# Kernel optimization log

Measured on AMD Instinct MI355X. Metric: run time of the kernel, lower is better.

Reference implementation:

```python
import jax, jax.numpy as jnp
import numpy as np

B, T, I, H, O = 64, 512, 512, 1024, 128
EPS = 1e-5

def _uniform(key, shape, bound):
    return jax.random.uniform(key, shape, jnp.float32, -bound, bound)

def setup_inputs() -> dict:
    key = jax.random.key(0)
    ks = jax.random.split(key, 16)
    bI = 1.0 / np.sqrt(I)
    bH = 1.0 / np.sqrt(H)
    inp = {
        "x": jax.random.normal(ks[0], (B, T, I), jnp.float32),
        # input projection (Linear: y = x @ W.T + b)
        "w_proj": _uniform(ks[1], (H, I), bI),
        "b_proj": _uniform(ks[2], (H,), bI),
        # GRU layer 0 (input_dim -> hidden_dim), PyTorch gate order [r, z, n]
        "w_ih0": _uniform(ks[3], (3 * H, I), bH),
        "w_hh0": _uniform(ks[4], (3 * H, H), bH),
        "b_ih0": _uniform(ks[5], (3 * H,), bH),
        "b_hh0": _uniform(ks[6], (3 * H,), bH),
        # GRU layer 1 (hidden_dim -> hidden_dim)
        "w_ih1": _uniform(ks[7], (3 * H, H), bH),
        "w_hh1": _uniform(ks[8], (3 * H, H), bH),
        "b_ih1": _uniform(ks[9], (3 * H,), bH),
        "b_hh1": _uniform(ks[10], (3 * H,), bH),
        # BatchNorm1d (eval mode: running stats)
        "bn_gamma": jnp.ones((H,), jnp.float32),
        "bn_beta": jnp.zeros((H,), jnp.float32),
        "bn_mean": jnp.zeros((H,), jnp.float32),
        "bn_var": jnp.ones((H,), jnp.float32),
        # output projection
        "w_out": _uniform(ks[11], (O, H), bH),
        "b_out": _uniform(ks[12], (O,), bH),
    }
    return inp

def _gru_layer(x_seq, w_ih, w_hh, b_ih, b_hh):
    """x_seq: [B, T, D_in] -> outputs [B, T, H]. PyTorch GRU gate math."""
    # Precompute input-side gates for all timesteps in one big GEMM.
    gx = jnp.einsum('btd,gd->btg', x_seq, w_ih) + b_ih      # [B, T, 3H]
    gx = jnp.transpose(gx, (1, 0, 2))                        # [T, B, 3H]
    h0 = jnp.zeros((x_seq.shape[0], w_hh.shape[1]), x_seq.dtype)

    def step(h, gx_t):
        gh = h @ w_hh.T + b_hh                               # [B, 3H]
        gxr, gxz, gxn = jnp.split(gx_t, 3, axis=-1)
        ghr, ghz, ghn = jnp.split(gh, 3, axis=-1)
        r = jax.nn.sigmoid(gxr + ghr)
        z = jax.nn.sigmoid(gxz + ghz)
        n = jnp.tanh(gxn + r * ghn)
        h_new = (1.0 - z) * n + z * h
        return h_new, h_new

    _, ys = jax.lax.scan(step, h0, gx)                       # ys: [T, B, H]
    return jnp.transpose(ys, (1, 0, 2))                      # [B, T, H]

def reference(x, w_proj, b_proj,
              w_ih0, w_hh0, b_ih0, b_hh0,
              w_ih1, w_hh1, b_ih1, b_hh1,
              bn_gamma, bn_beta, bn_mean, bn_var,
              w_out, b_out):
    x_projected = x @ w_proj.T + b_proj                      # [B, T, H]
    h1 = _gru_layer(x, w_ih0, w_hh0, b_ih0, b_hh0)           # layer 0
    gru_out = _gru_layer(h1, w_ih1, w_hh1, b_ih1, b_hh1)     # layer 1 (eval: no inter-layer dropout)
    residual = x_projected + gru_out
    out = residual[:, -1, :]                                 # [B, H]
    # BatchNorm1d in eval mode (running stats); dropout is identity in eval.
    out = (out - bn_mean) * jax.lax.rsqrt(bn_var + EPS) * bn_gamma + bn_beta
    out = out @ w_out.T + b_out                              # [B, O]
    return out
```

## Files before the change

kernel.cpp:

```cpp
#include <hip/hip_runtime.h>
#include <math.h>

#define BB 64
#define TT 512
#define II 512
#define HH 1024
#define OO 128
#define GN (3*HH)
#define TC 64
#define NCH (TT/TC)

using u16 = unsigned short;
typedef __attribute__((ext_vector_type(8))) short bf16x8;
typedef __attribute__((ext_vector_type(4))) float f32x4;
typedef __attribute__((ext_vector_type(4))) unsigned short u16x4;
typedef __attribute__((ext_vector_type(2))) unsigned long long u64x2;

__device__ __forceinline__ u16 f2bf(float f){
  unsigned u = __builtin_bit_cast(unsigned, f);
  u += 0x7fffu + ((u >> 16) & 1u);
  return (u16)(u >> 16);
}
__device__ __forceinline__ float bf2f(u16 h){
  unsigned u = ((unsigned)h) << 16;
  return __builtin_bit_cast(float, u);
}

__global__ __launch_bounds__(256) void cvt_kernel(const float* __restrict__ s,
                                                  u16* __restrict__ d, int n4){
  int stride = gridDim.x * 256;
  for (int i = blockIdx.x * 256 + threadIdx.x; i < n4; i += stride){
    float4 v = reinterpret_cast<const float4*>(s)[i];
    u16x4 o; o.x = f2bf(v.x); o.y = f2bf(v.y); o.z = f2bf(v.z); o.w = f2bf(v.w);
    reinterpret_cast<u16x4*>(d)[i] = o;
  }
}

__global__ __launch_bounds__(256) void cvtx_chunk(const float* __restrict__ x,
                                                  u16* __restrict__ d, int t0){
  const int per_b = TC * II / 4;
  int stride = gridDim.x * 256;
  for (int i = blockIdx.x * 256 + threadIdx.x; i < BB * per_b; i += stride){
    int b = i / per_b, r = i - b * per_b;
    float4 v = reinterpret_cast<const float4*>(x)[(size_t)(b * TT + t0) * (II/4) + r];
    u16x4 o; o.x = f2bf(v.x); o.y = f2bf(v.y); o.z = f2bf(v.z); o.w = f2bf(v.w);
    reinterpret_cast<u16x4*>(d)[(size_t)b * per_b + r] = o;
  }
}

template<int K>
__global__ __launch_bounds__(256) void gemm_bias(const u16* __restrict__ A,
    const u16* __restrict__ Bw, const float* __restrict__ bias, u16* __restrict__ C){
  __shared__ u16 As[128*32];
  __shared__ u16 Bs[128*32];
  int tid = threadIdx.x;
  int lane = tid & 63, wave = tid >> 6;
  int m0 = blockIdx.x * 128, n0 = blockIdx.y * 128;
  int wr = (wave >> 1) * 64, wc = (wave & 1) * 64;
  int fr = lane & 15, fo = (lane >> 4) * 8;
  f32x4 acc[4][4] = {};
  for (int k0 = 0; k0 < K; k0 += 32){
    __syncthreads();
    #pragma unroll
    for (int c = 0; c < 2; ++c){
      int chunk = wave * 2 + c;
      int s = chunk * 64 + lane;
      int row = s >> 2, o = s & 3;
      const u16* ga = A  + (size_t)(m0 + row) * K + k0 + o * 8;
      const u16* gb = Bw + (size_t)(n0 + row) * K + k0 + o * 8;
      __builtin_amdgcn_global_load_lds(
          (const __attribute__((address_space(1))) unsigned int*)ga,
          (__attribute__((address_space(3))) unsigned int*)(As + chunk * 512), 16, 0, 0);
      __builtin_amdgcn_global_load_lds(
          (const __attribute__((address_space(1))) unsigned int*)gb,
          (__attribute__((address_space(3))) unsigned int*)(Bs + chunk * 512), 16, 0, 0);
    }
    __syncthreads();
    bf16x8 af[4], bf[4];
    #pragma unroll
    for (int m = 0; m < 4; ++m)
      af[m] = *reinterpret_cast<const bf16x8*>(&As[(wr + m*16 + fr) * 32 + fo]);
    #pragma unroll
    for (int n = 0; n < 4; ++n)
      bf[n] = *reinterpret_cast<const bf16x8*>(&Bs[(wc + n*16 + fr) * 32 + fo]);
    #pragma unroll
    for (int m = 0; m < 4; ++m)
      #pragma unroll
      for (int n = 0; n < 4; ++n)
        acc[m][n] = __builtin_amdgcn_mfma_f32_16x16x32_bf16(af[m], bf[n], acc[m][n], 0, 0, 0);
  }
  int r4 = (lane >> 4) * 4;
  #pragma unroll
  for (int n = 0; n < 4; ++n){
    int col = n0 + wc + n*16 + fr;
    float bv = bias[col];
    #pragma unroll
    for (int m = 0; m < 4; ++m){
      #pragma unroll
      for (int q = 0; q < 4; ++q){
        int row = m0 + wr + m*16 + r4 + q;
        C[(size_t)row * GN + col] = f2bf(acc[m][n][q] + bv);
      }
    }
  }
}

__device__ __forceinline__ void gru_chunk(
    const u16* __restrict__ gx, const u16* __restrict__ Whh, const float* __restrict__ bhh,
    u16* hbuf, unsigned* flags, u16* h1c, float* hstate,
    int bl, u16* Ws, float* part, float* bsh)
{
  int tid = threadIdx.x, lane = tid & 63, w = tid >> 6;
  int g = bl >> 6, wg = bl & 63;
  int c0 = wg * 16, rb0 = g * 32;
  for (int ch = tid; ch < 48 * 128; ch += 256){
    int r = ch >> 7, o = ch & 127;
    const u16* src = Whh + (size_t)((r >> 4) * HH + c0 + (r & 15)) * HH + o * 8;
    *reinterpret_cast<int4*>(&Ws[r * 1032 + o * 8]) = *reinterpret_cast<const int4*>(src);
  }
  if (tid < 48) bsh[tid] = bhh[(tid >> 4) * HH + c0 + (tid & 15)];
  __syncthreads();
  int b2 = tid >> 4, j = tid & 15;
  int fr = lane & 15, klo = (lane >> 4) * 8, kw = w * 256;
  const u16* gxp0 = gx + (size_t)(rb0 + b2) * TC * GN + c0 + j;
  const u16* gxp1 = gx + (size_t)(rb0 + 16 + b2) * TC * GN + c0 + j;
  unsigned* fgrp = flags + g * 1024;
  float ho0 = hstate[(size_t)(rb0 + b2) * HH + c0 + j];
  float ho1 = hstate[(size_t)(rb0 + 16 + b2) * HH + c0 + j];
  int lnD = (b2 >> 2) * 16 + j, regD = b2 & 3;
  float br = bhh[c0 + j];
  int par = 0;
  for (int tl = 0; tl < TC; ++tl){
    float gxr0 = bf2f(gxp0[(size_t)tl * GN]);
    float gxz0 = bf2f(gxp0[(size_t)tl * GN + HH]);
    float gxn0 = bf2f(gxp0[(size_t)tl * GN + 2 * HH]);
    float gxr1 = bf2f(gxp1[(size_t)tl * GN]);
    float gxz1 = bf2f(gxp1[(size_t)tl * GN + HH]);
    float gxn1 = bf2f(gxp1[(size_t)tl * GN + 2 * HH]);
    if (tl){
      for (;;){
        unsigned v = __hip_atomic_load(fgrp + lane * 16, __ATOMIC_RELAXED,
                                       __HIP_MEMORY_SCOPE_AGENT);
        if (__all((int)(v >= (unsigned)tl))) break;
        __builtin_amdgcn_s_sleep(1);
      }
    }
    asm volatile("" ::: "memory");
    const u16* hr0 = hbuf + (size_t)par * (BB*HH) + (size_t)(rb0 + fr) * HH + kw + klo;
    const u16* hr1 = hr0 + (size_t)16 * HH;
    unsigned long long a0lo[8], a0hi[8], a1lo[8], a1hi[8];
    #pragma unroll
    for (int ks = 0; ks < 8; ++ks){
      a0lo[ks] = __hip_atomic_load((const unsigned long long*)(hr0 + ks * 32),
                                   __ATOMIC_RELAXED, __HIP_MEMORY_SCOPE_AGENT);
      a0hi[ks] = __hip_atomic_load((const unsigned long long*)(hr0 + ks * 32 + 4),
                                   __ATOMIC_RELAXED, __HIP_MEMORY_SCOPE_AGENT);
      a1lo[ks] = __hip_atomic_load((const unsigned long long*)(hr1 + ks * 32),
                                   __ATOMIC_RELAXED, __HIP_MEMORY_SCOPE_AGENT);
      a1hi[ks] = __hip_atomic_load((const unsigned long long*)(hr1 + ks * 32 + 4),
                                   __ATOMIC_RELAXED, __HIP_MEMORY_SCOPE_AGENT);
    }
    f32x4 acc[2][3] = {};
    #pragma unroll
    for (int ks = 0; ks < 8; ++ks){
      int kk = kw + ks * 32 + klo;
      bf16x8 w0 = *reinterpret_cast<const bf16x8*>(&Ws[(      fr) * 1032 + kk]);
      bf16x8 w1 = *reinterpret_cast<const bf16x8*>(&Ws[(16 + fr) * 1032 + kk]);
      bf16x8 w2 = *reinterpret_cast<const bf16x8*>(&Ws[(32 + fr) * 1032 + kk]);
      u64x2 p0; p0.x = a0lo[ks]; p0.y = a0hi[ks];
      bf16x8 af0 = __builtin_bit_cast(bf16x8, p0);
      acc[0][0] = __builtin_amdgcn_mfma_f32_16x16x32_bf16(af0, w0, acc[0][0], 0, 0, 0);
      acc[0][1] = __builtin_amdgcn_mfma_f32_16x16x32_bf16(af0, w1, acc[0][1], 0, 0, 0);
      acc[0][2] = __builtin_amdgcn_mfma_f32_16x16x32_bf16(af0, w2, acc[0][2], 0, 0, 0);
      u64x2 p1; p1.x = a1lo[ks]; p1.y = a1hi[ks];
      bf16x8 af1 = __builtin_bit_cast(bf16x8, p1);
      acc[1][0] = __builtin_amdgcn_mfma_f32_16x16x32_bf16(af1, w0, acc[1][0], 0, 0, 0);
      acc[1][1] = __builtin_amdgcn_mfma_f32_16x16x32_bf16(af1, w1, acc[1][1], 0, 0, 0);
      acc[1][2] = __builtin_amdgcn_mfma_f32_16x16x32_bf16(af1, w2, acc[1][2], 0, 0, 0);
    }
    #pragma unroll
    for (int at = 0; at < 2; ++at)
      #pragma unroll
      for (int gt = 0; gt < 3; ++gt)
        *reinterpret_cast<f32x4*>(&part[((w*6 + at*3 + gt)*64 + lane)*4]) = acc[at][gt];
    __syncthreads();
    float gh[2][3];
    #pragma unroll
    for (int at = 0; at < 2; ++at)
      #pragma unroll
      for (int gt = 0; gt < 3; ++gt){
        float s = 0.f;
        #pragma unroll
        for (int ww = 0; ww < 4; ++ww)
          s += part[((ww*6 + at*3 + gt)*64 + lnD)*4 + regD];
        gh[at][gt] = s;
      }
    float bz = bsh[16 + j], bn2 = bsh[32 + j];
    float r0 = __builtin_amdgcn_rcpf(1.f + __expf(-(gxr0 + gh[0][0] + br)));
    float z0 = __builtin_amdgcn_rcpf(1.f + __expf(-(gxz0 + gh[0][1] + bz)));
    float nx0 = gxn0 + r0 * (gh[0][2] + bn2);
    float n0 = 1.f - 2.f * __builtin_amdgcn_rcpf(__expf(2.f * nx0) + 1.f);
    float hn0 = (1.f - z0) * n0 + z0 * ho0;
    float r1 = __builtin_amdgcn_rcpf(1.f + __expf(-(gxr1 + gh[1][0] + br)));
    float z1 = __builtin_amdgcn_rcpf(1.f + __expf(-(gxz1 + gh[1][1] + bz)));
    float nx1 = gxn1 + r1 * (gh[1][2] + bn2);
    float n1 = 1.f - 2.f * __builtin_amdgcn_rcpf(__expf(2.f * nx1) + 1.f);
    float hn1 = (1.f - z1) * n1 + z1 * ho1;
    ho0 = hn0; ho1 = hn1;
    u16 hb0 = f2bf(hn0), hb1 = f2bf(hn1);
    size_t d0 = (size_t)(par ^ 1) * (BB*HH) + (size_t)(rb0 + b2) * HH + c0 + j;
    __hip_atomic_store(hbuf + d0,               hb0, __ATOMIC_RELAXED, __HIP_MEMORY_SCOPE_AGENT);
    __hip_atomic_store(hbuf + d0 + (size_t)16*HH, hb1, __ATOMIC_RELAXED, __HIP_MEMORY_SCOPE_AGENT);
    if (h1c){
      h1c[((size_t)(rb0 + b2) * TC + tl) * HH + c0 + j] = hb0;
      h1c[((size_t)(rb0 + 16 + b2) * TC + tl) * HH + c0 + j] = hb1;
    }
    if (tl == TC - 1){
      hstate[(size_t)(rb0 + b2) * HH + c0 + j] = hn0;
      hstate[(size_t)(rb0 + 16 + b2) * HH + c0 + j] = hn1;
    }
    __syncthreads();
    if (tid == 0)
      __hip_atomic_store(fgrp + wg * 16, (unsigned)(tl + 1), __ATOMIC_RELAXED,
                         __HIP_MEMORY_SCOPE_AGENT);
    par ^= 1;
  }
}

__global__ __launch_bounds__(256, 1) void gru_fused(
    const u16* gxA, const u16* WhhA, const float* bhhA, u16* hbufA,
    unsigned* flA, u16* h1cA, float* hstA,
    const u16* gxB, const u16* WhhB, const float* bhhB, u16* hbufB,
    unsigned* flB, float* hstB)
{
  __shared__ u16 Ws[48 * 1032];
  __shared__ float part[4*6*64*4];
  __shared__ float bsh[48];
  int blk = blockIdx.x;
  if (blk < 128){
    if (!gxA) return;
    gru_chunk(gxA, WhhA, bhhA, hbufA, flA, h1cA, hstA, blk, Ws, part, bsh);
  } else {
    if (!gxB) return;
    gru_chunk(gxB, WhhB, bhhB, hbufB, flB, nullptr, hstB, blk - 128, Ws, part, bsh);
  }
}

__global__ __launch_bounds__(256) void xproj_kernel(const float* __restrict__ x,
    const float* __restrict__ wproj, const float* __restrict__ bproj, float* __restrict__ xp){
  __shared__ float xs[II];
  int b = blockIdx.x >> 2, n0 = (blockIdx.x & 3) << 8;
  const float* xrow = x + ((size_t)b * TT + (TT - 1)) * II;
  for (int i = threadIdx.x; i < II; i += 256) xs[i] = xrow[i];
  __syncthreads();
  int n = n0 + threadIdx.x;
  const float* wrow = wproj + (size_t)n * II;
  float s = 0.f;
  #pragma unroll 4
  for (int k = 0; k < II; k += 4){
    float4 w4 = *reinterpret_cast<const float4*>(&wrow[k]);
    s += xs[k]*w4.x + xs[k+1]*w4.y + xs[k+2]*w4.z + xs[k+3]*w4.w;
  }
  xp[(size_t)b * HH + n] = s + bproj[n];
}

__global__ __launch_bounds__(256) void final_kernel(const float* __restrict__ xp,
    const float* __restrict__ hl, const float* __restrict__ gamma, const float* __restrict__ beta,
    const float* __restrict__ mean, const float* __restrict__ var,
    const float* __restrict__ wout, const float* __restrict__ bout, float* __restrict__ out){
  __shared__ float bn[2 * HH];
  int b0 = blockIdx.x * 2;
  for (int i = threadIdx.x; i < 2 * HH; i += 256){
    int bb = i >> 10, jj = i & (HH - 1);
    float res = xp[(size_t)(b0 + bb) * HH + jj] + hl[(size_t)(b0 + bb) * HH + jj];
    bn[i] = (res - mean[jj]) * rsqrtf(var[jj] + 1e-5f) * gamma[jj] + beta[jj];
  }
  __syncthreads();
  int bb = threadIdx.x >> 7, o = threadIdx.x & (OO - 1);
  const float* wrow = wout + (size_t)o * HH;
  const float* bnrow = bn + bb * HH;
  float s = 0.f;
  #pragma unroll 4
  for (int k = 0; k < HH; k += 4){
    float4 w4 = *reinterpret_cast<const float4*>(&wrow[k]);
    s += bnrow[k]*w4.x + bnrow[k+1]*w4.y + bnrow[k+2]*w4.z + bnrow[k+3]*w4.w;
  }
  out[(size_t)(b0 + bb) * OO + o] = s + bout[o];
}

extern "C" void kernel_launch(void* const* d_in, const int* in_sizes, int n_in,
                              void* d_out, int out_size, void* d_ws, size_t ws_size,
                              hipStream_t stream) {
  const float* x      = (const float*)d_in[0];
  const float* w_proj = (const float*)d_in[1];
  const float* b_proj = (const float*)d_in[2];
  const float* w_ih0  = (const float*)d_in[3];
  const float* w_hh0  = (const float*)d_in[4];
  const float* b_ih0  = (const float*)d_in[5];
  const float* b_hh0  = (const float*)d_in[6];
  const float* w_ih1  = (const float*)d_in[7];
  const float* w_hh1  = (const float*)d_in[8];
  const float* b_ih1  = (const float*)d_in[9];
  const float* b_hh1  = (const float*)d_in[10];
  const float* gamma  = (const float*)d_in[11];
  const float* beta   = (const float*)d_in[12];
  const float* mean   = (const float*)d_in[13];
  const float* var    = (const float*)d_in[14];
  const float* w_out  = (const float*)d_in[15];
  const float* b_out  = (const float*)d_in[16];
  float* out = (float*)d_out;

  char* ws = (char*)d_ws;
  size_t off = 0;
  unsigned* flags = (unsigned*)(ws + off); off += (size_t)18 * 2048 * 4;
  u16* hbuf0   = (u16*)(ws + off);   off += (size_t)2*BB*HH*2;
  u16* hbuf1   = (u16*)(ws + off);   off += (size_t)2*BB*HH*2;
  float* hst0  = (float*)(ws + off); off += (size_t)BB*HH*4;
  float* hst1  = (float*)(ws + off); off += (size_t)BB*HH*4;
  size_t zero_bytes = off;
  float* xproj = (float*)(ws + off); off += (size_t)BB*HH*4;
  u16* xck     = (u16*)(ws + off);   off += (size_t)BB*TC*II*2;
  u16* h1c     = (u16*)(ws + off);   off += (size_t)BB*TC*HH*2;
  u16* wih0b   = (u16*)(ws + off);   off += (size_t)3*HH*II*2;
  u16* whh0b   = (u16*)(ws + off);   off += (size_t)3*HH*HH*2;
  u16* wih1b   = (u16*)(ws + off);   off += (size_t)3*HH*HH*2;
  u16* whh1b   = (u16*)(ws + off);   off += (size_t)3*HH*HH*2;
  u16* gxc0    = (u16*)(ws + off);   off += (size_t)BB*TC*3*HH*2;
  u16* gxc1    = (u16*)(ws + off);   off += (size_t)BB*TC*3*HH*2;

  hipMemsetAsync(d_ws, 0, zero_bytes, stream);

  cvt_kernel<<<512, 256, 0, stream>>>(w_ih0, wih0b, (3*HH*II) / 4);
  cvt_kernel<<<512, 256, 0, stream>>>(w_hh0, whh0b, (3*HH*HH) / 4);
  cvt_kernel<<<512, 256, 0, stream>>>(w_ih1, wih1b, (3*HH*HH) / 4);
  cvt_kernel<<<512, 256, 0, stream>>>(w_hh1, whh1b, (3*HH*HH) / 4);

  xproj_kernel<<<256, 256, 0, stream>>>(x, w_proj, b_proj, xproj);

  dim3 ggrid(BB * TC / 128, GN / 128);
  auto fl = [&](int k, int role){ return flags + (size_t)(k*2 + role) * 2048; };

  cvtx_chunk<<<1024, 256, 0, stream>>>(x, xck, 0);
  gemm_bias<II><<<ggrid, 256, 0, stream>>>(xck, wih0b, b_ih0, gxc0);
  gru_fused<<<256, 256, 0, stream>>>(gxc0, whh0b, b_hh0, hbuf0, fl(0,0), h1c, hst0,
                                     nullptr, whh1b, b_hh1, hbuf1, fl(0,1), hst1);
  for (int k = 1; k < NCH; ++k){
    gemm_bias<HH><<<ggrid, 256, 0, stream>>>(h1c, wih1b, b_ih1, gxc1);
    cvtx_chunk<<<1024, 256, 0, stream>>>(x, xck, k * TC);
    gemm_bias<II><<<ggrid, 256, 0, stream>>>(xck, wih0b, b_ih0, gxc0);
    gru_fused<<<256, 256, 0, stream>>>(gxc0, whh0b, b_hh0, hbuf0, fl(k,0), h1c, hst0,
                                       gxc1, whh1b, b_hh1, hbuf1, fl(k,1), hst1);
  }
  gemm_bias<HH><<<ggrid, 256, 0, stream>>>(h1c, wih1b, b_ih1, gxc1);
  gru_fused<<<256, 256, 0, stream>>>(nullptr, whh0b, b_hh0, hbuf0, fl(8,0), h1c, hst0,
                                     gxc1, whh1b, b_hh1, hbuf1, fl(8,1), hst1);

  final_kernel<<<BB / 2, 256, 0, stream>>>(xproj, hst1, gamma, beta, mean, var, w_out, b_out, out);
}
```

Before: 3.675 ms.

## Use a per-timestep ring of hidden-state slots so recurrent reads are plain vector loads

Replaces the two-slot ping-pong hidden-state buffer with a 66-slot ring indexed by global timestep. Slot 0 stays zero and serves as the initial state. Because each step within a launch reads an address that has not been touched earlier in that launch, the 64-bit atomic loads become ordinary 16-byte vector loads. This is meant to cut load-instruction count and latency on the serial critical path. The cost is a much larger workspace, and correctness now relies on the cache behaviour of non-atomic loads on never-before-read addresses.

```diff
diff --git a/kernel.cpp b/kernel.cpp
--- a/kernel.cpp
+++ b/kernel.cpp
@@ -9,12 +9,12 @@
 #define GN (3*HH)
 #define TC 64
 #define NCH (TT/TC)
+#define NSLOT 66
 
 using u16 = unsigned short;
 typedef __attribute__((ext_vector_type(8))) short bf16x8;
 typedef __attribute__((ext_vector_type(4))) float f32x4;
 typedef __attribute__((ext_vector_type(4))) unsigned short u16x4;
-typedef __attribute__((ext_vector_type(2))) unsigned long long u64x2;
 
 __device__ __forceinline__ u16 f2bf(float f){
   unsigned u = __builtin_bit_cast(unsigned, f);
@@ -107,7 +107,7 @@
 
 __device__ __forceinline__ void gru_chunk(
     const u16* __restrict__ gx, const u16* __restrict__ Whh, const float* __restrict__ bhh,
-    u16* hbuf, unsigned* flags, u16* h1c, float* hstate,
+    u16* hbuf, unsigned* flags, u16* h1c, float* hstate, int base,
     int bl, u16* Ws, float* part, float* bsh)
 {
   int tid = threadIdx.x, lane = tid & 63, w = tid >> 6;
@@ -129,8 +129,8 @@
   float ho1 = hstate[(size_t)(rb0 + 16 + b2) * HH + c0 + j];
   int lnD = (b2 >> 2) * 16 + j, regD = b2 & 3;
   float br = bhh[c0 + j];
-  int par = 0;
   for (int tl = 0; tl < TC; ++tl){
+    int t = base + tl;
     float gxr0 = bf2f(gxp0[(size_t)tl * GN]);
     float gxz0 = bf2f(gxp0[(size_t)tl * GN + HH]);
     float gxn0 = bf2f(gxp0[(size_t)tl * GN + 2 * HH]);
@@ -146,19 +146,14 @@
       }
     }
     asm volatile("" ::: "memory");
-    const u16* hr0 = hbuf + (size_t)par * (BB*HH) + (size_t)(rb0 + fr) * HH + kw + klo;
+    const u16* rslot = hbuf + (size_t)(((t - 1) % 65) + 1) * (BB * HH);
+    const u16* hr0 = rslot + (size_t)(rb0 + fr) * HH + kw + klo;
     const u16* hr1 = hr0 + (size_t)16 * HH;
-    unsigned long long a0lo[8], a0hi[8], a1lo[8], a1hi[8];
+    bf16x8 af0[8], af1[8];
     #pragma unroll
     for (int ks = 0; ks < 8; ++ks){
-      a0lo[ks] = __hip_atomic_load((const unsigned long long*)(hr0 + ks * 32),
-                                   __ATOMIC_RELAXED, __HIP_MEMORY_SCOPE_AGENT);
-      a0hi[ks] = __hip_atomic_load((const unsigned long long*)(hr0 + ks * 32 + 4),
-                                   __ATOMIC_RELAXED, __HIP_MEMORY_SCOPE_AGENT);
-      a1lo[ks] = __hip_atomic_load((const unsigned long long*)(hr1 + ks * 32),
-                                   __ATOMIC_RELAXED, __HIP_MEMORY_SCOPE_AGENT);
-      a1hi[ks] = __hip_atomic_load((const unsigned long long*)(hr1 + ks * 32 + 4),
-                                   __ATOMIC_RELAXED, __HIP_MEMORY_SCOPE_AGENT);
+      af0[ks] = *reinterpret_cast<const bf16x8*>(hr0 + ks * 32);
+      af1[ks] = *reinterpret_cast<const bf16x8*>(hr1 + ks * 32);
     }
     f32x4 acc[2][3] = {};
     #pragma unroll
@@ -167,16 +162,12 @@
       bf16x8 w0 = *reinterpret_cast<const bf16x8*>(&Ws[(      fr) * 1032 + kk]);
       bf16x8 w1 = *reinterpret_cast<const bf16x8*>(&Ws[(16 + fr) * 1032 + kk]);
       bf16x8 w2 = *reinterpret_cast<const bf16x8*>(&Ws[(32 + fr) * 1032 + kk]);
-      u64x2 p0; p0.x = a0lo[ks]; p0.y = a0hi[ks];
-      bf16x8 af0 = __builtin_bit_cast(bf16x8, p0);
-      acc[0][0] = __builtin_amdgcn_mfma_f32_16x16x32_bf16(af0, w0, acc[0][0], 0, 0, 0);
-      acc[0][1] = __builtin_amdgcn_mfma_f32_16x16x32_bf16(af0, w1, acc[0][1], 0, 0, 0);
-      acc[0][2] = __builtin_amdgcn_mfma_f32_16x16x32_bf16(af0, w2, acc[0][2], 0, 0, 0);
-      u64x2 p1; p1.x = a1lo[ks]; p1.y = a1hi[ks];
-      bf16x8 af1 = __builtin_bit_cast(bf16x8, p1);
-      acc[1][0] = __builtin_amdgcn_mfma_f32_16x16x32_bf16(af1, w0, acc[1][0], 0, 0, 0);
-      acc[1][1] = __builtin_amdgcn_mfma_f32_16x16x32_bf16(af1, w1, acc[1][1], 0, 0, 0);
-      acc[1][2] = __builtin_amdgcn_mfma_f32_16x16x32_bf16(af1, w2, acc[1][2], 0, 0, 0);
+      acc[0][0] = __builtin_amdgcn_mfma_f32_16x16x32_bf16(af0[ks], w0, acc[0][0], 0, 0, 0);
+      acc[0][1] = __builtin_amdgcn_mfma_f32_16x16x32_bf16(af0[ks], w1, acc[0][1], 0, 0, 0);
+      acc[0][2] = __builtin_amdgcn_mfma_f32_16x16x32_bf16(af0[ks], w2, acc[0][2], 0, 0, 0);
+      acc[1][0] = __builtin_amdgcn_mfma_f32_16x16x32_bf16(af1[ks], w0, acc[1][0], 0, 0, 0);
+      acc[1][1] = __builtin_amdgcn_mfma_f32_16x16x32_bf16(af1[ks], w1, acc[1][1], 0, 0, 0);
+      acc[1][2] = __builtin_amdgcn_mfma_f32_16x16x32_bf16(af1[ks], w2, acc[1][2], 0, 0, 0);
     }
     #pragma unroll
     for (int at = 0; at < 2; ++at)
@@ -208,9 +199,10 @@
     float hn1 = (1.f - z1) * n1 + z1 * ho1;
     ho0 = hn0; ho1 = hn1;
     u16 hb0 = f2bf(hn0), hb1 = f2bf(hn1);
-    size_t d0 = (size_t)(par ^ 1) * (BB*HH) + (size_t)(rb0 + b2) * HH + c0 + j;
-    __hip_atomic_store(hbuf + d0,               hb0, __ATOMIC_RELAXED, __HIP_MEMORY_SCOPE_AGENT);
-    __hip_atomic_store(hbuf + d0 + (size_t)16*HH, hb1, __ATOMIC_RELAXED, __HIP_MEMORY_SCOPE_AGENT);
+    u16* wslot = hbuf + (size_t)((t % 65) + 1) * (BB * HH);
+    size_t d0 = (size_t)(rb0 + b2) * HH + c0 + j;
+    __hip_atomic_store(wslot + d0,                hb0, __ATOMIC_RELAXED, __HIP_MEMORY_SCOPE_AGENT);
+    __hip_atomic_store(wslot + d0 + (size_t)16*HH, hb1, __ATOMIC_RELAXED, __HIP_MEMORY_SCOPE_AGENT);
     if (h1c){
       h1c[((size_t)(rb0 + b2) * TC + tl) * HH + c0 + j] = hb0;
       h1c[((size_t)(rb0 + 16 + b2) * TC + tl) * HH + c0 + j] = hb1;
@@ -223,15 +215,14 @@
     if (tid == 0)
       __hip_atomic_store(fgrp + wg * 16, (unsigned)(tl + 1), __ATOMIC_RELAXED,
                          __HIP_MEMORY_SCOPE_AGENT);
-    par ^= 1;
   }
 }
 
 __global__ __launch_bounds__(256, 1) void gru_fused(
     const u16* gxA, const u16* WhhA, const float* bhhA, u16* hbufA,
-    unsigned* flA, u16* h1cA, float* hstA,
+    unsigned* flA, u16* h1cA, float* hstA, int baseA,
     const u16* gxB, const u16* WhhB, const float* bhhB, u16* hbufB,
-    unsigned* flB, float* hstB)
+    unsigned* flB, float* hstB, int baseB)
 {
   __shared__ u16 Ws[48 * 1032];
   __shared__ float part[4*6*64*4];
@@ -239,10 +230,10 @@
   int blk = blockIdx.x;
   if (blk < 128){
     if (!gxA) return;
-    gru_chunk(gxA, WhhA, bhhA, hbufA, flA, h1cA, hstA, blk, Ws, part, bsh);
+    gru_chunk(gxA, WhhA, bhhA, hbufA, flA, h1cA, hstA, baseA, blk, Ws, part, bsh);
   } else {
     if (!gxB) return;
-    gru_chunk(gxB, WhhB, bhhB, hbufB, flB, nullptr, hstB, blk - 128, Ws, part, bsh);
+    gru_chunk(gxB, WhhB, bhhB, hbufB, flB, nullptr, hstB, baseB, blk - 128, Ws, part, bsh);
   }
 }
 
@@ -313,11 +304,11 @@
   char* ws = (char*)d_ws;
   size_t off = 0;
   unsigned* flags = (unsigned*)(ws + off); off += (size_t)18 * 2048 * 4;
-  u16* hbuf0   = (u16*)(ws + off);   off += (size_t)2*BB*HH*2;
-  u16* hbuf1   = (u16*)(ws + off);   off += (size_t)2*BB*HH*2;
   float* hst0  = (float*)(ws + off); off += (size_t)BB*HH*4;
   float* hst1  = (float*)(ws + off); off += (size_t)BB*HH*4;
-  size_t zero_bytes = off;
+  size_t zeroA = off;
+  u16* hbuf0   = (u16*)(ws + off);   off += (size_t)NSLOT*BB*HH*2;
+  u16* hbuf1   = (u16*)(ws + off);   off += (size_t)NSLOT*BB*HH*2;
   float* xproj = (float*)(ws + off); off += (size_t)BB*HH*4;
   u16* xck     = (u16*)(ws + off);   off += (size_t)BB*TC*II*2;
   u16* h1c     = (u16*)(ws + off);   off += (size_t)BB*TC*HH*2;
@@ -328,7 +319,9 @@
   u16* gxc0    = (u16*)(ws + off);   off += (size_t)BB*TC*3*HH*2;
   u16* gxc1    = (u16*)(ws + off);   off += (size_t)BB*TC*3*HH*2;
 
-  hipMemsetAsync(d_ws, 0, zero_bytes, stream);
+  hipMemsetAsync(d_ws, 0, zeroA, stream);
+  hipMemsetAsync(hbuf0, 0, (size_t)BB*HH*2, stream);
+  hipMemsetAsync(hbuf1, 0, (size_t)BB*HH*2, stream);
 
   cvt_kernel<<<512, 256, 0, stream>>>(w_ih0, wih0b, (3*HH*II) / 4);
   cvt_kernel<<<512, 256, 0, stream>>>(w_hh0, whh0b, (3*HH*HH) / 4);
@@ -342,18 +335,18 @@
 
   cvtx_chunk<<<1024, 256, 0, stream>>>(x, xck, 0);
   gemm_bias<II><<<ggrid, 256, 0, stream>>>(xck, wih0b, b_ih0, gxc0);
-  gru_fused<<<256, 256, 0, stream>>>(gxc0, whh0b, b_hh0, hbuf0, fl(0,0), h1c, hst0,
-                                     nullptr, whh1b, b_hh1, hbuf1, fl(0,1), hst1);
+  gru_fused<<<256, 256, 0, stream>>>(gxc0, whh0b, b_hh0, hbuf0, fl(0,0), h1c, hst0, 0,
+                                     nullptr, whh1b, b_hh1, hbuf1, fl(0,1), hst1, 0);
   for (int k = 1; k < NCH; ++k){
     gemm_bias<HH><<<ggrid, 256, 0, stream>>>(h1c, wih1b, b_ih1, gxc1);
     cvtx_chunk<<<1024, 256, 0, stream>>>(x, xck, k * TC);
     gemm_bias<II><<<ggrid, 256, 0, stream>>>(xck, wih0b, b_ih0, gxc0);
-    gru_fused<<<256, 256, 0, stream>>>(gxc0, whh0b, b_hh0, hbuf0, fl(k,0), h1c, hst0,
-                                       gxc1, whh1b, b_hh1, hbuf1, fl(k,1), hst1);
+    gru_fused<<<256, 256, 0, stream>>>(gxc0, whh0b, b_hh0, hbuf0, fl(k,0), h1c, hst0, k*TC,
+                                       gxc1, whh1b, b_hh1, hbuf1, fl(k,1), hst1, (k-1)*TC);
   }
   gemm_bias<HH><<<ggrid, 256, 0, stream>>>(h1c, wih1b, b_ih1, gxc1);
-  gru_fused<<<256, 256, 0, stream>>>(nullptr, whh0b, b_hh0, hbuf0, fl(8,0), h1c, hst0,
-                                     gxc1, whh1b, b_hh1, hbuf1, fl(8,1), hst1);
+  gru_fused<<<256, 256, 0, stream>>>(nullptr, whh0b, b_hh0, hbuf0, fl(8,0), h1c, hst0, 0,
+                                     gxc1, whh1b, b_hh1, hbuf1, fl(8,1), hst1, (NCH-1)*TC);
 
   final_kernel<<<BB / 2, 256, 0, stream>>>(xproj, hst1, gamma, beta, mean, var, w_out, b_out, out);
 }
```

Result: faster. 3.070 ms (-16.5%).
